# Kernel optimization log

Measured on AMD Instinct MI355X. Metric: run time of the kernel, lower is better.

The kernel has to match this reference:

```python
import jax, jax.numpy as jnp
import numpy as np

M = 4096          # output features (n_rows, c_3)
H = 4096          # input features  (n_cols, c_4)
NNZ_PER_ROW = 2048
NNZ = M * NNZ_PER_ROW
B, S = 4, 2048    # batch, seq -> flattened to N = B*S row-vecs in the original loop


def setup_inputs() -> dict:
    key = jax.random.key(0)
    k1, k2, k3 = jax.random.split(key, 3)
    x = jax.random.normal(k1, (B, S, H), jnp.float32)
    values = jax.random.normal(k2, (NNZ,), jnp.float32) * 0.02
    # unique, sorted column indices per row (valid CSR structure)
    scores = jax.random.uniform(k3, (M, H))
    cols = jnp.argsort(scores, axis=1)[:, :NNZ_PER_ROW].astype(jnp.int32)
    col_idx = jnp.sort(cols, axis=1).reshape(-1)
    row_ptr = (jnp.arange(M + 1, dtype=jnp.int32) * NNZ_PER_ROW)
    return {"x": x, "values": values, "col_idx": col_idx, "row_ptr": row_ptr}


def _decode_csr(values, col_idx, row_ptr, n_rows, n_cols):
    """Decode compressed (CSR) weight once into dense [n_rows, n_cols]."""
    nnz = values.shape[0]
    row_ids = jnp.searchsorted(row_ptr, jnp.arange(nnz, dtype=row_ptr.dtype), side='right') - 1
    W = jnp.zeros((n_rows, n_cols), values.dtype).at[row_ids, col_idx].add(values)
    return W


def reference(x, values, col_idx, row_ptr):
    # Original loops macko_spmv.multiply over each flattened row of x:
    #   out_flat[i] = W_sparse @ x_flat[i]
    # Fused/batched equivalent: decode the compressed weight once, single GEMM.
    W = _decode_csr(values, col_idx, row_ptr, M, H)     # [M, H]
    out = jnp.einsum('bsh,mh->bsm', x, W)               # [B, S, M]
    return out
```

## Files before the change

### kernel.cpp

```cpp
#include <hip/hip_runtime.h>

#define H_DIM   4096
#define M_DIM   4096
#define N_ROWS  8192
#define NNZ_ROW 2048
#define NT      (H_DIM / 64)

typedef __bf16 bf16x8 __attribute__((ext_vector_type(8)));
typedef float  f32x4  __attribute__((ext_vector_type(4)));

__device__ __forceinline__ unsigned short f2bf(float f) {
    unsigned int u = __float_as_uint(f);
    u += 0x7fffu + ((u >> 16) & 1u);
    return (unsigned short)(u >> 16);
}

__device__ __forceinline__ void gld_lds16(const void* g, void* l) {
    __builtin_amdgcn_global_load_lds(
        (__attribute__((address_space(1))) const void*)g,
        (__attribute__((address_space(3))) void*)l,
        16, 0, 0);
}

__device__ __forceinline__ void wg_barrier() {
    __builtin_amdgcn_sched_barrier(0);
    asm volatile("" ::: "memory");
    __builtin_amdgcn_s_barrier();
    asm volatile("" ::: "memory");
    __builtin_amdgcn_sched_barrier(0);
}

#define LGKM0_FENCE() do { \
    asm volatile("s_waitcnt lgkmcnt(0)" ::: "memory"); \
    __builtin_amdgcn_sched_barrier(0); \
} while (0)

__global__ __launch_bounds__(256) void decode_w_kernel(
        const float* __restrict__ values,
        const int*   __restrict__ col_idx,
        unsigned short* __restrict__ W) {
    __shared__ unsigned short buf[4 * H_DIM];
    const int r4 = blockIdx.x;
    const int t  = threadIdx.x;

    uint4 z = make_uint4(0u, 0u, 0u, 0u);
    #pragma unroll
    for (int i = 0; i < 8; ++i) ((uint4*)buf)[i * 256 + t] = z;
    __syncthreads();

    #pragma unroll
    for (int rl = 0; rl < 4; ++rl) {
        const long base = ((long)(4 * r4 + rl)) * NNZ_ROW;
        #pragma unroll
        for (int j = 0; j < NNZ_ROW; j += 256) {
            float v = values[base + j + t];
            int   c = col_idx[base + j + t];
            buf[rl * H_DIM + c] = f2bf(v);
        }
    }
    __syncthreads();

    const long wbase = (long)(4 * r4) * H_DIM;
    #pragma unroll
    for (int it = 0; it < 8; ++it) {
        const int s = it * 256 + t;
        *(uint4*)&W[wbase + (long)s * 8] = *(const uint4*)&buf[s * 8];
    }
}

__global__ __launch_bounds__(256) void convert_x_kernel(
        const float4* __restrict__ x, unsigned long long* __restrict__ xb) {
    const long total = (long)N_ROWS * H_DIM / 4;
    for (long i = (long)blockIdx.x * 256 + threadIdx.x; i < total;
         i += (long)gridDim.x * 256) {
        float4 a = x[i];
        union { unsigned short s[4]; unsigned long long v; } r;
        r.s[0] = f2bf(a.x); r.s[1] = f2bf(a.y);
        r.s[2] = f2bf(a.z); r.s[3] = f2bf(a.w);
        xb[i] = r.v;
    }
}

__global__ __launch_bounds__(512, 2) void gemm256_kernel(
        const unsigned short* __restrict__ A,
        const unsigned short* __restrict__ B,
        float* __restrict__ C) {
    __shared__ unsigned short lds[2 * 32768];

    const int t    = threadIdx.x;
    const int lane = t & 63;
    const int wid  = t >> 6;
    const int wm   = wid >> 2;
    const int wn   = wid & 3;

    const int bid   = blockIdx.x;
    const int wg    = (bid & 7) * 64 + (bid >> 3);
    const int ctile = wg >> 5;
    const int rtile = wg & 31;
    const long row0 = (long)rtile * 256;
    const long col0 = (long)ctile * 256;

    const int rr = t >> 3;
    const int cc = ((t & 7) ^ (rr & 7)) * 8;
    const unsigned short* pA = A + (row0 + rr) * H_DIM + cc;
    const unsigned short* pB = B + (col0 + rr) * H_DIM + cc;
    unsigned short* const Ld = &lds[t * 8];

#define STAGE(bufo) do { \
    gld_lds16(pA,               Ld + (bufo));         \
    gld_lds16(pA +  64 * H_DIM, Ld + (bufo) + 4096);  \
    gld_lds16(pA + 128 * H_DIM, Ld + (bufo) + 8192);  \
    gld_lds16(pA + 192 * H_DIM, Ld + (bufo) + 12288); \
    gld_lds16(pB,               Ld + (bufo) + 16384); \
    gld_lds16(pB +  64 * H_DIM, Ld + (bufo) + 20480); \
    gld_lds16(pB + 128 * H_DIM, Ld + (bufo) + 24576); \
    gld_lds16(pB + 192 * H_DIM, Ld + (bufo) + 28672); \
    pA += 64; pB += 64; \
} while (0)

    const int fr = lane & 15;
    const int jq = lane >> 4;
    const int cx = fr & 7;
    const int off0 = ((0 * 4 + jq) ^ cx) * 8;
    const int off1 = ((1 * 4 + jq) ^ cx) * 8;
    const int aoff = wm * 8192 + fr * 64;
    const int boff = 16384 + (wn >> 1) * 8192 + ((wn & 1) * 64 + fr) * 64;

    f32x4 acc[8][4];
    #pragma unroll
    for (int i = 0; i < 8; ++i)
        #pragma unroll
        for (int j = 0; j < 4; ++j) acc[i][j] = (f32x4)0.0f;

    auto TILE = [&](const int cb) {
        const unsigned short* Ab = &lds[cb + aoff];
        const unsigned short* Bb = &lds[cb + boff];
        bf16x8 a[4][2], b0[2][2], b1[2][2];
        #pragma unroll
        for (int i = 0; i < 4; ++i) {
            a[i][0] = *(const bf16x8*)(Ab + i * 1024 + off0);
            a[i][1] = *(const bf16x8*)(Ab + i * 1024 + off1);
        }
        #pragma unroll
        for (int j = 0; j < 2; ++j) {
            b0[j][0] = *(const bf16x8*)(Bb + j * 1024 + off0);
            b0[j][1] = *(const bf16x8*)(Bb + j * 1024 + off1);
        }
        LGKM0_FENCE();
        __builtin_amdgcn_s_setprio(1);
        #pragma unroll
        for (int i = 0; i < 4; ++i)
            #pragma unroll
            for (int j = 0; j < 2; ++j) {
                acc[i][j] = __builtin_amdgcn_mfma_f32_16x16x32_bf16(
                                a[i][0], b0[j][0], acc[i][j], 0, 0, 0);
                acc[i][j] = __builtin_amdgcn_mfma_f32_16x16x32_bf16(
                                a[i][1], b0[j][1], acc[i][j], 0, 0, 0);
            }
        __builtin_amdgcn_s_setprio(0);
        #pragma unroll
        for (int j = 0; j < 2; ++j) {
            b1[j][0] = *(const bf16x8*)(Bb + (2 + j) * 1024 + off0);
            b1[j][1] = *(const bf16x8*)(Bb + (2 + j) * 1024 + off1);
        }
        LGKM0_FENCE();
        __builtin_amdgcn_s_setprio(1);
        #pragma unroll
        for (int i = 0; i < 4; ++i)
            #pragma unroll
            for (int j = 0; j < 2; ++j) {
                acc[i][2 + j] = __builtin_amdgcn_mfma_f32_16x16x32_bf16(
                                    a[i][0], b1[j][0], acc[i][2 + j], 0, 0, 0);
                acc[i][2 + j] = __builtin_amdgcn_mfma_f32_16x16x32_bf16(
                                    a[i][1], b1[j][1], acc[i][2 + j], 0, 0, 0);
            }
        __builtin_amdgcn_s_setprio(0);
        #pragma unroll
        for (int i = 0; i < 4; ++i) {
            a[i][0] = *(const bf16x8*)(Ab + (4 + i) * 1024 + off0);
            a[i][1] = *(const bf16x8*)(Ab + (4 + i) * 1024 + off1);
        }
        LGKM0_FENCE();
        __builtin_amdgcn_s_setprio(1);
        #pragma unroll
        for (int i = 0; i < 4; ++i)
            #pragma unroll
            for (int j = 0; j < 2; ++j) {
                acc[4 + i][2 + j] = __builtin_amdgcn_mfma_f32_16x16x32_bf16(
                                        a[i][0], b1[j][0], acc[4 + i][2 + j], 0, 0, 0);
                acc[4 + i][2 + j] = __builtin_amdgcn_mfma_f32_16x16x32_bf16(
                                        a[i][1], b1[j][1], acc[4 + i][2 + j], 0, 0, 0);
            }
        __builtin_amdgcn_s_setprio(0);
        __builtin_amdgcn_s_setprio(1);
        #pragma unroll
        for (int i = 0; i < 4; ++i)
            #pragma unroll
            for (int j = 0; j < 2; ++j) {
                acc[4 + i][j] = __builtin_amdgcn_mfma_f32_16x16x32_bf16(
                                    a[i][0], b0[j][0], acc[4 + i][j], 0, 0, 0);
                acc[4 + i][j] = __builtin_amdgcn_mfma_f32_16x16x32_bf16(
                                    a[i][1], b0[j][1], acc[4 + i][j], 0, 0, 0);
            }
        __builtin_amdgcn_s_setprio(0);
    };

    STAGE(0);
    #pragma unroll 1
    for (int kt = 0; kt < NT - 2; kt += 2) {
        STAGE(32768);
        asm volatile("s_waitcnt vmcnt(8)" ::: "memory");
        wg_barrier();
        TILE(0);
        wg_barrier();
        STAGE(0);
        asm volatile("s_waitcnt vmcnt(8)" ::: "memory");
        wg_barrier();
        TILE(32768);
        wg_barrier();
    }
    STAGE(32768);
    asm volatile("s_waitcnt vmcnt(8)" ::: "memory");
    wg_barrier();
    TILE(0);
    wg_barrier();
    asm volatile("s_waitcnt vmcnt(0)" ::: "memory");
    wg_barrier();
    TILE(32768);

#undef STAGE

    const int dcol = lane & 15;
    const int dr4  = (lane >> 4) * 4;
    const long crow = row0 + wm * 128;
    const int  ccol = (int)col0 + wn * 64 + dcol;
    #pragma unroll
    for (int i = 0; i < 8; ++i) {
        float* cp = C + (crow + i * 16 + dr4) * M_DIM + ccol;
        #pragma unroll
        for (int j = 0; j < 4; ++j)
            #pragma unroll
            for (int q = 0; q < 4; ++q)
                cp[(long)q * M_DIM + j * 16] = acc[i][j][q];
    }
}

__global__ __launch_bounds__(256) void naive_kernel(
        const float* __restrict__ x, const float* __restrict__ vals,
        const int* __restrict__ cols, float* __restrict__ out) {
    const long idx = blockIdx.x * 256L + threadIdx.x;
    const int  m   = (int)(idx & (M_DIM - 1));
    const long n   = idx >> 12;
    const float* xr = x + n * H_DIM;
    const float* v  = vals + (long)m * NNZ_ROW;
    const int*   c  = cols + (long)m * NNZ_ROW;
    float s = 0.f;
    for (int j = 0; j < NNZ_ROW; ++j) s += v[j] * xr[c[j]];
    out[idx] = s;
}

extern "C" void kernel_launch(void* const* d_in, const int* in_sizes, int n_in,
                              void* d_out, int out_size, void* d_ws, size_t ws_size,
                              hipStream_t stream) {
    const float* x       = (const float*)d_in[0];
    const float* values  = (const float*)d_in[1];
    const int*   col_idx = (const int*)d_in[2];
    float* out = (float*)d_out;

    const size_t wbytes = (size_t)M_DIM * H_DIM * sizeof(unsigned short);
    const size_t xbytes = (size_t)N_ROWS * H_DIM * sizeof(unsigned short);

    if (ws_size >= wbytes + xbytes) {
        unsigned short* Wd = (unsigned short*)d_ws;
        unsigned short* Xb = (unsigned short*)((char*)d_ws + wbytes);

        decode_w_kernel<<<M_DIM / 4, 256, 0, stream>>>(values, col_idx, Wd);
        convert_x_kernel<<<4096, 256, 0, stream>>>(
            (const float4*)x, (unsigned long long*)Xb);
        gemm256_kernel<<<512, 512, 0, stream>>>(Xb, Wd, out);
    } else {
        naive_kernel<<<(int)((long)N_ROWS * M_DIM / 256), 256, 0, stream>>>(
            x, values, col_idx, out);
    }
}
```

Baseline: 499.5 us.

## Interleave global-to-LDS prefetch of next-next K tile into MFMA phases

Restructures the bf16 GEMM main loop so loads for tile kt+2 are issued in pieces into the same LDS buffer while tile kt is being consumed, gated by extra workgroup barriers. Loads are spread across the four MFMA sub-phases instead of issued as one batch before each tile. The goal is finer-grained overlap of global loads with compute and a deeper prefetch distance. In exchange it adds many more barriers per tile, and correctness depends on the LDS regions being fully read before they are overwritten.

New measurement: 494.1 us. No clear change (-1.1%).

```diff
diff --git a/kernel.cpp b/kernel.cpp
--- a/kernel.cpp
+++ b/kernel.cpp
@@ -32,6 +32,11 @@
 
 #define LGKM0_FENCE() do { \
     asm volatile("s_waitcnt lgkmcnt(0)" ::: "memory"); \
+    __builtin_amdgcn_sched_barrier(0); \
+} while (0)
+
+#define VMCNT(n) do { \
+    asm volatile("s_waitcnt vmcnt(" #n ")" ::: "memory"); \
     __builtin_amdgcn_sched_barrier(0); \
 } while (0)
 
@@ -102,20 +107,23 @@
 
     const int rr = t >> 3;
     const int cc = ((t & 7) ^ (rr & 7)) * 8;
-    const unsigned short* pA = A + (row0 + rr) * H_DIM + cc;
-    const unsigned short* pB = B + (col0 + rr) * H_DIM + cc;
+    const unsigned short* pA_ = A + (row0 + rr) * H_DIM + cc;
+    const unsigned short* pB_ = B + (col0 + rr) * H_DIM + cc;
     unsigned short* const Ld = &lds[t * 8];
 
-#define STAGE(bufo) do { \
-    gld_lds16(pA,               Ld + (bufo));         \
-    gld_lds16(pA +  64 * H_DIM, Ld + (bufo) + 4096);  \
-    gld_lds16(pA + 128 * H_DIM, Ld + (bufo) + 8192);  \
-    gld_lds16(pA + 192 * H_DIM, Ld + (bufo) + 12288); \
-    gld_lds16(pB,               Ld + (bufo) + 16384); \
-    gld_lds16(pB +  64 * H_DIM, Ld + (bufo) + 20480); \
-    gld_lds16(pB + 128 * H_DIM, Ld + (bufo) + 24576); \
-    gld_lds16(pB + 192 * H_DIM, Ld + (bufo) + 28672); \
-    pA += 64; pB += 64; \
+#define SAE(kt, bo) do {  \
+    gld_lds16(pA_ + (long)(kt) * 64,               Ld + (bo));        \
+    gld_lds16(pA_ + (long)(kt) * 64 + 128 * H_DIM, Ld + (bo) + 8192); \
+} while (0)
+#define SAO(kt, bo) do {  \
+    gld_lds16(pA_ + (long)(kt) * 64 +  64 * H_DIM, Ld + (bo) + 4096);  \
+    gld_lds16(pA_ + (long)(kt) * 64 + 192 * H_DIM, Ld + (bo) + 12288); \
+} while (0)
+#define SBALL(kt, bo) do {  \
+    gld_lds16(pB_ + (long)(kt) * 64,               Ld + (bo) + 16384); \
+    gld_lds16(pB_ + (long)(kt) * 64 +  64 * H_DIM, Ld + (bo) + 20480); \
+    gld_lds16(pB_ + (long)(kt) * 64 + 128 * H_DIM, Ld + (bo) + 24576); \
+    gld_lds16(pB_ + (long)(kt) * 64 + 192 * H_DIM, Ld + (bo) + 28672); \
 } while (0)
 
     const int fr = lane & 15;
@@ -132,103 +140,92 @@
         #pragma unroll
         for (int j = 0; j < 4; ++j) acc[i][j] = (f32x4)0.0f;
 
-    auto TILE = [&](const int cb) {
-        const unsigned short* Ab = &lds[cb + aoff];
-        const unsigned short* Bb = &lds[cb + boff];
-        bf16x8 a[4][2], b0[2][2], b1[2][2];
+    bf16x8 a[4][2], b0[2][2], b1[2][2];
+
+    auto rdA = [&](int cb, int base4) {
         #pragma unroll
         for (int i = 0; i < 4; ++i) {
-            a[i][0] = *(const bf16x8*)(Ab + i * 1024 + off0);
-            a[i][1] = *(const bf16x8*)(Ab + i * 1024 + off1);
+            a[i][0] = *(const bf16x8*)&lds[cb + aoff + (base4 + i) * 1024 + off0];
+            a[i][1] = *(const bf16x8*)&lds[cb + aoff + (base4 + i) * 1024 + off1];
         }
+    };
+    auto rdB = [&](int cb, int base2, bf16x8 (&b)[2][2]) {
         #pragma unroll
         for (int j = 0; j < 2; ++j) {
-            b0[j][0] = *(const bf16x8*)(Bb + j * 1024 + off0);
-            b0[j][1] = *(const bf16x8*)(Bb + j * 1024 + off1);
+            b[j][0] = *(const bf16x8*)&lds[cb + boff + (base2 + j) * 1024 + off0];
+            b[j][1] = *(const bf16x8*)&lds[cb + boff + (base2 + j) * 1024 + off1];
         }
-        LGKM0_FENCE();
+    };
+    auto mm = [&](bf16x8 (&b)[2][2], int ib, int jb) {
         __builtin_amdgcn_s_setprio(1);
         #pragma unroll
         for (int i = 0; i < 4; ++i)
             #pragma unroll
             for (int j = 0; j < 2; ++j) {
-                acc[i][j] = __builtin_amdgcn_mfma_f32_16x16x32_bf16(
-                                a[i][0], b0[j][0], acc[i][j], 0, 0, 0);
-                acc[i][j] = __builtin_amdgcn_mfma_f32_16x16x32_bf16(
-                                a[i][1], b0[j][1], acc[i][j], 0, 0, 0);
+                acc[ib + i][jb + j] = __builtin_amdgcn_mfma_f32_16x16x32_bf16(
+                    a[i][0], b[j][0], acc[ib + i][jb + j], 0, 0, 0);
+                acc[ib + i][jb + j] = __builtin_amdgcn_mfma_f32_16x16x32_bf16(
+                    a[i][1], b[j][1], acc[ib + i][jb + j], 0, 0, 0);
             }
         __builtin_amdgcn_s_setprio(0);
-        #pragma unroll
-        for (int j = 0; j < 2; ++j) {
-            b1[j][0] = *(const bf16x8*)(Bb + (2 + j) * 1024 + off0);
-            b1[j][1] = *(const bf16x8*)(Bb + (2 + j) * 1024 + off1);
-        }
-        LGKM0_FENCE();
-        __builtin_amdgcn_s_setprio(1);
-        #pragma unroll
-        for (int i = 0; i < 4; ++i)
-            #pragma unroll
-            for (int j = 0; j < 2; ++j) {
-                acc[i][2 + j] = __builtin_amdgcn_mfma_f32_16x16x32_bf16(
-                                    a[i][0], b1[j][0], acc[i][2 + j], 0, 0, 0);
-                acc[i][2 + j] = __builtin_amdgcn_mfma_f32_16x16x32_bf16(
-                                    a[i][1], b1[j][1], acc[i][2 + j], 0, 0, 0);
-            }
-        __builtin_amdgcn_s_setprio(0);
-        #pragma unroll
-        for (int i = 0; i < 4; ++i) {
-            a[i][0] = *(const bf16x8*)(Ab + (4 + i) * 1024 + off0);
-            a[i][1] = *(const bf16x8*)(Ab + (4 + i) * 1024 + off1);
-        }
-        LGKM0_FENCE();
-        __builtin_amdgcn_s_setprio(1);
-        #pragma unroll
-        for (int i = 0; i < 4; ++i)
-            #pragma unroll
-            for (int j = 0; j < 2; ++j) {
-                acc[4 + i][2 + j] = __builtin_amdgcn_mfma_f32_16x16x32_bf16(
-                                        a[i][0], b1[j][0], acc[4 + i][2 + j], 0, 0, 0);
-                acc[4 + i][2 + j] = __builtin_amdgcn_mfma_f32_16x16x32_bf16(
-                                        a[i][1], b1[j][1], acc[4 + i][2 + j], 0, 0, 0);
-            }
-        __builtin_amdgcn_s_setprio(0);
-        __builtin_amdgcn_s_setprio(1);
-        #pragma unroll
-        for (int i = 0; i < 4; ++i)
-            #pragma unroll
-            for (int j = 0; j < 2; ++j) {
-                acc[4 + i][j] = __builtin_amdgcn_mfma_f32_16x16x32_bf16(
-                                    a[i][0], b0[j][0], acc[4 + i][j], 0, 0, 0);
-                acc[4 + i][j] = __builtin_amdgcn_mfma_f32_16x16x32_bf16(
-                                    a[i][1], b0[j][1], acc[4 + i][j], 0, 0, 0);
-            }
-        __builtin_amdgcn_s_setprio(0);
-    };
-
-    STAGE(0);
+    };
+
+    auto tileMain = [&](int cb, int st) {
+        rdA(cb, 0); rdB(cb, 0, b0);
+        wg_barrier(); LGKM0_FENCE();
+        mm(b0, 0, 0);
+        wg_barrier();
+        rdB(cb, 2, b1);
+        SAE(st, cb);
+        wg_barrier(); LGKM0_FENCE();
+        mm(b1, 0, 2);
+        wg_barrier();
+        rdA(cb, 4);
+        SBALL(st, cb);
+        wg_barrier(); LGKM0_FENCE();
+        mm(b1, 4, 2);
+        wg_barrier();
+        SAO(st, cb);
+        VMCNT(8);
+        wg_barrier();
+        mm(b0, 4, 0);
+        wg_barrier();
+    };
+    auto tileLast = [&](int cb, bool drain) {
+        rdA(cb, 0); rdB(cb, 0, b0);
+        wg_barrier(); LGKM0_FENCE();
+        mm(b0, 0, 0);
+        wg_barrier();
+        rdB(cb, 2, b1);
+        wg_barrier(); LGKM0_FENCE();
+        mm(b1, 0, 2);
+        wg_barrier();
+        rdA(cb, 4);
+        wg_barrier(); LGKM0_FENCE();
+        mm(b1, 4, 2);
+        wg_barrier();
+        if (drain) VMCNT(0);
+        wg_barrier();
+        mm(b0, 4, 0);
+        wg_barrier();
+    };
+
+    SAE(0, 0); SAO(0, 0); SBALL(0, 0);
+    SAE(1, 32768); SAO(1, 32768); SBALL(1, 32768);
+    VMCNT(8);
+    wg_barrier();
+
     #pragma unroll 1
     for (int kt = 0; kt < NT - 2; kt += 2) {
-        STAGE(32768);
-        asm volatile("s_waitcnt vmcnt(8)" ::: "memory");
-        wg_barrier();
-        TILE(0);
-        wg_barrier();
-        STAGE(0);
-        asm volatile("s_waitcnt vmcnt(8)" ::: "memory");
-        wg_barrier();
-        TILE(32768);
-        wg_barrier();
-    }
-    STAGE(32768);
-    asm volatile("s_waitcnt vmcnt(8)" ::: "memory");
-    wg_barrier();
-    TILE(0);
-    wg_barrier();
-    asm volatile("s_waitcnt vmcnt(0)" ::: "memory");
-    wg_barrier();
-    TILE(32768);
-
-#undef STAGE
+        tileMain(0,     kt + 2);
+        tileMain(32768, kt + 3);
+    }
+    tileLast(0, true);
+    tileLast(32768, false);
+
+#undef SAE
+#undef SAO
+#undef SBALL
 
     const int dcol = lane & 15;
     const int dr4  = (lane >> 4) * 4;
```
